# Kernel optimization log

Hardware: AMD Instinct MI355X
Metric: run time of the kernel (lower is better)

The kernel has to match this reference:

```python
import jax, jax.numpy as jnp
import numpy as np
import math

B, S, H = 4, 1024, 1024
E, TOP_K, WINDOW = 4, 2, 64
CONFIGS = [(8, 'standard'), (12, 'standard'), (8, 'linear'), (8, 'local')]
PARAM_NAMES = ['Wq', 'bq', 'Wk', 'bk', 'Wv', 'bv', 'Wo', 'bo']


def setup_inputs() -> dict:
    key = jax.random.key(0)
    ks = jax.random.split(key, 2 + 8 * E)
    d = {}
    d['x'] = jax.random.normal(ks[0], (B, S, H), jnp.float32)
    d['Wg'] = jax.random.normal(ks[1], (H, E), jnp.float32) * 0.02
    i = 2
    for e, (nh, _) in enumerate(CONFIGS):
        hd = H // nh
        pd = nh * hd  # 1020 for nh=12, else 1024
        shapes = [(H, pd), (pd,), (H, pd), (pd,), (H, pd), (pd,), (pd, H), (H,)]
        for nm, shp in zip(PARAM_NAMES, shapes):
            d[f'e{e}_{nm}'] = jax.random.normal(ks[i], shp, jnp.float32) * 0.02
            i += 1
    d['attention_mask'] = jnp.ones((B, S), jnp.int32)
    return d


def _heads(y, nh, hd):
    b, s, _ = y.shape
    return y.reshape(b, s, nh, hd).transpose(0, 2, 1, 3)  # [b, nh, s, hd]


def _attention_expert(x, mask, Wq, bq, Wk, bk, Wv, bv, Wo, bo, nh, atype):
    b, s, _ = x.shape
    hd = Wq.shape[1] // nh
    scale = math.sqrt(hd)
    q = _heads(x @ Wq + bq, nh, hd)
    k = _heads(x @ Wk + bk, nh, hd)
    v = _heads(x @ Wv + bv, nh, hd)
    if atype == 'linear':
        # kernel-trick linear attention; original ignores attention_mask here
        q = jax.nn.elu(q) + 1.0
        k = jax.nn.elu(k) + 1.0
        kv = jnp.einsum('bhsd,bhse->bhde', k, v)
        num = jnp.einsum('bhqd,bhde->bhqe', q, kv)
        den = jnp.einsum('bhqd,bhd->bhq', q, k.sum(axis=2)) + 1e-6
        out = num / den[..., None]
    else:
        scores = jnp.einsum('bhqd,bhkd->bhqk', q, k) / scale
        if atype == 'local':
            idx = jnp.arange(s)
            dist = idx[None, :] - idx[:, None]  # j - i
            local_mask = jnp.abs(dist) <= WINDOW // 2
            scores = jnp.where(local_mask[None, None], scores, -jnp.inf)
        scores = jnp.where(mask[:, None, None, :] == 0, -jnp.inf, scores)
        probs = jax.nn.softmax(scores, axis=-1)
        probs = jnp.where(jnp.isnan(probs), 0.0, probs)  # nan_to_num(nan=0)
        out = jnp.einsum('bhqk,bhkd->bhqd', probs, v)
    out = out.transpose(0, 2, 1, 3).reshape(b, s, -1)
    return out @ Wo + bo


def _forward(x, Wg, eparams, attention_mask):
    b, s, h = x.shape
    # TopKGating (eval mode: no noise). logits -> top_k -> softmax over selected
    logits = x.reshape(-1, h) @ Wg  # [b*s, E]
    top_vals, top_idx = jax.lax.top_k(logits, TOP_K)
    gate_w = jax.nn.softmax(top_vals, axis=-1).reshape(b, s, TOP_K)
    sel = top_idx.reshape(b, s, TOP_K)
    outs = jnp.stack([
        _attention_expert(x, attention_mask, *eparams[e], CONFIGS[e][0], CONFIGS[e][1])
        for e in range(E)
    ], axis=0)  # [E, b, s, h]
    perm = outs.transpose(1, 2, 0, 3)  # [b, s, E, h]
    selected = jnp.take_along_axis(perm, sel[..., None], axis=2)  # [b, s, K, h]
    return (selected * gate_w[..., None]).sum(axis=2)


def reference(x, Wg,
              e0_Wq, e0_bq, e0_Wk, e0_bk, e0_Wv, e0_bv, e0_Wo, e0_bo,
              e1_Wq, e1_bq, e1_Wk, e1_bk, e1_Wv, e1_bv, e1_Wo, e1_bo,
              e2_Wq, e2_bq, e2_Wk, e2_bk, e2_Wv, e2_bv, e2_Wo, e2_bo,
              e3_Wq, e3_bq, e3_Wk, e3_bk, e3_Wv, e3_bv, e3_Wo, e3_bo,
              attention_mask):
    eparams = [
        (e0_Wq, e0_bq, e0_Wk, e0_bk, e0_Wv, e0_bv, e0_Wo, e0_bo),
        (e1_Wq, e1_bq, e1_Wk, e1_bk, e1_Wv, e1_bv, e1_Wo, e1_bo),
        (e2_Wq, e2_bq, e2_Wk, e2_bk, e2_Wv, e2_bv, e2_Wo, e2_bo),
        (e3_Wq, e3_bq, e3_Wk, e3_bk, e3_Wv, e3_bv, e3_Wo, e3_bo),
    ]
    return _forward(x, Wg, eparams, attention_mask)
```

## Files before the change

### kernel.cpp

```cpp
#include <hip/hip_runtime.h>
#include <cmath>

#define B_ 4
#define S_ 1024
#define H_ 1024

typedef short bf16x8 __attribute__((ext_vector_type(8)));
typedef float f32x4 __attribute__((ext_vector_type(4)));
typedef _Float16 half4 __attribute__((ext_vector_type(4)));

__device__ __forceinline__ unsigned short f2bf(float f) {
  unsigned u = __float_as_uint(f);
  u += 0x7fff + ((u >> 16) & 1);
  return (unsigned short)(u >> 16);
}
__device__ __forceinline__ float bf2f(unsigned short h) {
  return __uint_as_float(((unsigned)h) << 16);
}
__device__ __forceinline__ void gld16(const void* g, void* l) {
  __builtin_amdgcn_global_load_lds(
      (const __attribute__((address_space(1))) unsigned int*)g,
      (__attribute__((address_space(3))) unsigned int*)l, 16, 0, 0);
}

__global__ __launch_bounds__(64) void gate_kernel(
    const float* __restrict__ x, const float* __restrict__ Wg,
    float* __restrict__ gw) {
  int t = blockIdx.x;
  int lane = threadIdx.x;
  const float* xr = x + (size_t)t * H_;
  float a0 = 0.f, a1 = 0.f, a2 = 0.f, a3 = 0.f;
  for (int h = lane; h < H_; h += 64) {
    float xv = xr[h];
    const float* wr = Wg + h * 4;
    a0 += xv * wr[0]; a1 += xv * wr[1]; a2 += xv * wr[2]; a3 += xv * wr[3];
  }
  for (int off = 32; off > 0; off >>= 1) {
    a0 += __shfl_down(a0, off);
    a1 += __shfl_down(a1, off);
    a2 += __shfl_down(a2, off);
    a3 += __shfl_down(a3, off);
  }
  if (lane == 0) {
    float v[4] = {a0, a1, a2, a3};
    int i0 = 0; float b0 = v[0];
    for (int e = 1; e < 4; ++e) if (v[e] > b0) { b0 = v[e]; i0 = e; }
    int i1 = -1; float b1 = -INFINITY;
    for (int e = 0; e < 4; ++e) { if (e == i0) continue; if (v[e] > b1) { b1 = v[e]; i1 = e; } }
    float e1v = expf(b1 - b0);
    float w0 = 1.f / (1.f + e1v);
    float w1 = e1v / (1.f + e1v);
    float o[4] = {0.f, 0.f, 0.f, 0.f};
    o[i0] = w0; o[i1] = w1;
    float* g = gw + t * 4;
    g[0] = o[0]; g[1] = o[1]; g[2] = o[2]; g[3] = o[3];
  }
}

__global__ __launch_bounds__(256) void conv_kernel(
    const float* __restrict__ src, unsigned short* __restrict__ dst,
    int nsrc, int ldsrc) {
  int idx = blockIdx.x * 256 + threadIdx.x;
  int m = idx >> 10, c = idx & 1023;
  dst[idx] = (c < nsrc) ? f2bf(src[(size_t)m * ldsrc + c]) : (unsigned short)0;
}

__global__ __launch_bounds__(256) void wtrans4_kernel(
    const float* __restrict__ s0, const float* __restrict__ s1,
    const float* __restrict__ s2, const float* __restrict__ s3,
    unsigned short* __restrict__ d0, unsigned short* __restrict__ d1,
    unsigned short* __restrict__ d2, unsigned short* __restrict__ d3, int pd) {
  __shared__ float tile[32][33];
  int z = blockIdx.z;
  const float* src = (z == 0) ? s0 : (z == 1) ? s1 : (z == 2) ? s2 : s3;
  unsigned short* dst = (z == 0) ? d0 : (z == 1) ? d1 : (z == 2) ? d2 : d3;
  int ksrc = (z < 3) ? 1024 : pd;
  int nsrc = (z < 3) ? pd : 1024;
  int ldsrc = (z < 3) ? pd : 1024;
  int k0 = blockIdx.x * 32, n0 = blockIdx.y * 32;
  int tx = threadIdx.x & 31, ty = threadIdx.x >> 5;
  for (int i = 0; i < 32; i += 8) {
    int k = k0 + ty + i, n = n0 + tx;
    tile[ty + i][tx] = (k < ksrc && n < nsrc) ? src[(size_t)k * ldsrc + n] : 0.f;
  }
  __syncthreads();
  for (int i = 0; i < 32; i += 8) {
    int n = n0 + ty + i, k = k0 + tx;
    dst[(size_t)n * 1024 + k] = f2bf(tile[tx][ty + i]);
  }
}

__global__ __launch_bounds__(256) void gemm_mfma(
    const unsigned short* __restrict__ A, const unsigned short* __restrict__ Bt,
    const float* __restrict__ b0, const float* __restrict__ b1,
    const float* __restrict__ b2, void* __restrict__ Cv, int ldc,
    int nact, int elu_ncut, int out_bf16, int mode,
    const float* __restrict__ gw, int expert, int remap,
    int qs_ncut, float qscale) {
  constexpr int K = 1024;
  __shared__ __align__(16) unsigned short As[128 * 32];
  __shared__ __align__(16) unsigned short Bs[128 * 32];
  int tid = threadIdx.x, wave = tid >> 6, lane = tid & 63;
  int quad = lane >> 4, lrow = lane & 15;
  int rw = (wave >> 1) * 64, cw = (wave & 1) * 64;
  int m0 = blockIdx.y * 128, n0 = blockIdx.x * 128;
  int srow = wave * 32 + (lane >> 2);
  int scol = (lane & 3) * 8;
  const unsigned short* gA = A + (size_t)(m0 + srow) * K + scol;
  const unsigned short* gB = Bt + (size_t)(n0 + srow) * K + scol;
  unsigned short* lA = &As[wave * 1024];
  unsigned short* lB = &Bs[wave * 1024];
  f32x4 acc[4][4];
#pragma unroll
  for (int mt = 0; mt < 4; ++mt)
#pragma unroll
    for (int nt = 0; nt < 4; ++nt) acc[mt][nt] = (f32x4){0.f, 0.f, 0.f, 0.f};

  for (int k0 = 0; k0 < K; k0 += 32) {
    gld16(gA + k0, lA);
    gld16(gA + 16 * K + k0, lA + 512);
    gld16(gB + k0, lB);
    gld16(gB + 16 * K + k0, lB + 512);
    __syncthreads();
    bf16x8 af[4], bfr[4];
#pragma unroll
    for (int t = 0; t < 4; ++t) {
      af[t]  = *(const bf16x8*)&As[(rw + t * 16 + lrow) * 32 + quad * 8];
      bfr[t] = *(const bf16x8*)&Bs[(cw + t * 16 + lrow) * 32 + quad * 8];
    }
#pragma unroll
    for (int mt = 0; mt < 4; ++mt)
#pragma unroll
      for (int nt = 0; nt < 4; ++nt)
        acc[mt][nt] = __builtin_amdgcn_mfma_f32_16x16x32_bf16(
            af[mt], bfr[nt], acc[mt][nt], 0, 0, 0);
    __syncthreads();
  }
#pragma unroll
  for (int nt = 0; nt < 4; ++nt) {
    int n = n0 + cw + nt * 16 + lrow;
    int slice = n >> 10, noff = n & 1023;
    if (noff >= nact) continue;
    const float* bp = (slice == 0) ? b0 : (slice == 1) ? b1 : b2;
    float bias = bp[noff];
    bool do_elu = n < elu_ncut;
    bool do_qs = n < qs_ncut;
    int col = n;
    if (remap) {
      int head = (noff * 12337) >> 20;
      col = slice * 1152 + head * 96 + (noff - head * 85);
    }
#pragma unroll
    for (int mt = 0; mt < 4; ++mt) {
      int mb = m0 + rw + mt * 16 + quad * 4;
#pragma unroll
      for (int r = 0; r < 4; ++r) {
        int m = mb + r;
        float val = acc[mt][nt][r] + bias;
        if (do_elu) val = (val > 0.f) ? val + 1.f : expf(val);
        if (do_qs) val *= qscale;
        size_t ci = (size_t)m * ldc + col;
        if (out_bf16) {
          ((unsigned short*)Cv)[ci] = f2bf(val);
        } else {
          float* C = (float*)Cv;
          if (mode == 0) C[ci] = val;
          else {
            float g = gw[m * 4 + expert];
            if (mode == 1) C[ci] = g * val;
            else           C[ci] += g * val;
          }
        }
      }
    }
  }
}

struct OutP {
  const unsigned short* A[4];
  const unsigned short* B[4];
  const float* bias[4];
};

__global__ __launch_bounds__(256) void gemm_out4(
    OutP p, const float* __restrict__ gw, float* __restrict__ part) {
  constexpr int K = 1024;
  __shared__ __align__(16) unsigned short As[128 * 32];
  __shared__ __align__(16) unsigned short Bs[128 * 32];
  int e = blockIdx.z;
  const unsigned short* A = p.A[e];
  const unsigned short* Bt = p.B[e];
  const float* bp = p.bias[e];
  float* C = part + (size_t)e * (4096ull * 1024ull);
  int tid = threadIdx.x, wave = tid >> 6, lane = tid & 63;
  int quad = lane >> 4, lrow = lane & 15;
  int rw = (wave >> 1) * 64, cw = (wave & 1) * 64;
  int m0 = blockIdx.y * 128, n0 = blockIdx.x * 128;
  int srow = wave * 32 + (lane >> 2);
  int scol = (lane & 3) * 8;
  const unsigned short* gA = A + (size_t)(m0 + srow) * K + scol;
  const unsigned short* gB = Bt + (size_t)(n0 + srow) * K + scol;
  unsigned short* lA = &As[wave * 1024];
  unsigned short* lB = &Bs[wave * 1024];
  f32x4 acc[4][4];
#pragma unroll
  for (int mt = 0; mt < 4; ++mt)
#pragma unroll
    for (int nt = 0; nt < 4; ++nt) acc[mt][nt] = (f32x4){0.f, 0.f, 0.f, 0.f};

  for (int k0 = 0; k0 < K; k0 += 32) {
    gld16(gA + k0, lA);
    gld16(gA + 16 * K + k0, lA + 512);
    gld16(gB + k0, lB);
    gld16(gB + 16 * K + k0, lB + 512);
    __syncthreads();
    bf16x8 af[4], bfr[4];
#pragma unroll
    for (int t = 0; t < 4; ++t) {
      af[t]  = *(const bf16x8*)&As[(rw + t * 16 + lrow) * 32 + quad * 8];
      bfr[t] = *(const bf16x8*)&Bs[(cw + t * 16 + lrow) * 32 + quad * 8];
    }
#pragma unroll
    for (int mt = 0; mt < 4; ++mt)
#pragma unroll
      for (int nt = 0; nt < 4; ++nt)
        acc[mt][nt] = __builtin_amdgcn_mfma_f32_16x16x32_bf16(
            af[mt], bfr[nt], acc[mt][nt], 0, 0, 0);
    __syncthreads();
  }
#pragma unroll
  for (int nt = 0; nt < 4; ++nt) {
    int n = n0 + cw + nt * 16 + lrow;
    float bias = bp[n];
#pragma unroll
    for (int mt = 0; mt < 4; ++mt) {
      int mb = m0 + rw + mt * 16 + quad * 4;
#pragma unroll
      for (int r = 0; r < 4; ++r) {
        int m = mb + r;
        float g = gw[m * 4 + e];
        C[(size_t)m * 1024 + n] = g * (acc[mt][nt][r] + bias);
      }
    }
  }
}

__global__ __launch_bounds__(256) void reduce4(
    const float* __restrict__ part, float* __restrict__ out) {
  constexpr size_t N = 4096ull * 1024ull;
  size_t idx = ((size_t)blockIdx.x * 256 + threadIdx.x) * 4;
  f32x4 a0 = *(const f32x4*)(part + idx);
  f32x4 a1 = *(const f32x4*)(part + idx + N);
  f32x4 a2 = *(const f32x4*)(part + idx + 2 * N);
  f32x4 a3 = *(const f32x4*)(part + idx + 3 * N);
  f32x4 s;
#pragma unroll
  for (int j = 0; j < 4; ++j) {
    float t = a0[j];
    t += a1[j]; t += a2[j]; t += a3[j];
    s[j] = t;
  }
  *(f32x4*)(out + idx) = s;
}

__global__ __launch_bounds__(256) void padzero(
    unsigned short* __restrict__ qkv1, unsigned short* __restrict__ aob1) {
  int idx = blockIdx.x * 256 + threadIdx.x;
  int m = idx / 396, r = idx % 396;
  int slice = r / 132, r2 = r % 132;
  int head = r2 / 11, c = 85 + r2 % 11;
  qkv1[(size_t)m * 3456 + slice * 1152 + head * 96 + c] = 0;
  if (idx < 4096 * 4) {
    int mm = idx >> 2, cc = 1020 + (idx & 3);
    aob1[(size_t)mm * 1024 + cc] = 0;
  }
}

template <int HD, bool LOCAL>
__device__ __forceinline__ void attn_body(
    char* smem,
    const unsigned short* __restrict__ q, const unsigned short* __restrict__ k,
    const unsigned short* __restrict__ v, const int* __restrict__ amask,
    unsigned short* __restrict__ ao, int ldq, int h) {
  constexpr int HDP = (HD + 31) & ~31;
  constexpr int DCH = HDP / 32;
  constexpr int NDT = HDP / 16;
  constexpr int NCH = HDP / 8;
  constexpr int QT = 256, KT = 64;
  constexpr int KLD = HDP + 8;
  constexpr int VLD = KT + 4;
  constexpr int W2 = 32;
  unsigned short* Ks = (unsigned short*)smem;
  _Float16* Vt = (_Float16*)(smem + (size_t)KT * KLD * 2);
  unsigned long long* amq =
      (unsigned long long*)(smem + (size_t)KT * KLD * 2 + (size_t)HDP * VLD * 2);
  int tid = threadIdx.x, wave = tid >> 6, lane = tid & 63;
  int quad = lane >> 4, l15 = lane & 15;
  int q0 = blockIdx.x * QT, b = blockIdx.z;
  size_t baseq = ((size_t)b * S_) * ldq + (size_t)h * HDP;
  size_t baseo = ((size_t)b * S_) * H_ + (size_t)h * HD;

  {
    unsigned long long bb0 = __ballot(amask[b * S_ + wave * 128 + lane] != 0);
    unsigned long long bb1 = __ballot(amask[b * S_ + wave * 128 + 64 + lane] != 0);
    if (lane == 0) { amq[wave * 2] = bb0; amq[wave * 2 + 1] = bb1; }
  }

  int qrow[2];
  bf16x8 qf[2][DCH];
#pragma unroll
  for (int g = 0; g < 2; ++g) {
    qrow[g] = q0 + wave * 32 + g * 16 + l15;
#pragma unroll
    for (int c = 0; c < DCH; ++c)
#pragma unroll
      for (int j = 0; j < 8; ++j) {
        int d = c * 32 + quad * 8 + j;
        qf[g][c][j] =
            (d < HD) ? (short)q[baseq + (size_t)qrow[g] * ldq + d] : (short)0;
      }
  }

  int jlo = 0, jhi = S_;
  if (LOCAL) {
    jlo = q0 - W2; if (jlo < 0) jlo = 0; jlo &= ~(KT - 1);
    jhi = q0 + QT + W2; if (jhi > S_) jhi = S_;
  }

  int skey = tid & 63, sc8a = tid >> 6, sc8b = 8 + (tid >> 6);
  bool sactb = sc8b < NCH;
  const unsigned short* kg = k + baseq + (size_t)skey * ldq;
  const unsigned short* vg = v + baseq + (size_t)skey * ldq;
  bf16x8 kra = {}, krb = {}, vra = {}, vrb = {};
  {
    size_t o = (size_t)jlo * ldq;
    kra = *(const bf16x8*)(kg + o + sc8a * 8);
    vra = *(const bf16x8*)(vg + o + sc8a * 8);
    if (sactb) {
      krb = *(const bf16x8*)(kg + o + sc8b * 8);
      vrb = *(const bf16x8*)(vg + o + sc8b * 8);
    }
  }

  float m_run[2] = {-1e30f, -1e30f}, l_run[2] = {0.f, 0.f};
  f32x4 accd[2][NDT];
#pragma unroll
  for (int g = 0; g < 2; ++g)
#pragma unroll
    for (int dt = 0; dt < NDT; ++dt) accd[g][dt] = (f32x4){0.f, 0.f, 0.f, 0.f};

  for (int j0 = jlo; j0 < jhi; j0 += KT) {
    __syncthreads();
    *(bf16x8*)&Ks[skey * KLD + sc8a * 8] = kra;
#pragma unroll
    for (int j = 0; j < 8; ++j)
      Vt[(sc8a * 8 + j) * VLD + skey] = (_Float16)bf2f((unsigned short)vra[j]);
    if (sactb) {
      *(bf16x8*)&Ks[skey * KLD + sc8b * 8] = krb;
#pragma unroll
      for (int j = 0; j < 8; ++j)
        Vt[(sc8b * 8 + j) * VLD + skey] = (_Float16)bf2f((unsigned short)vrb[j]);
    }
    __syncthreads();
    int jn = j0 + KT;
    if (jn < jhi) {
      size_t o = (size_t)jn * ldq;
      kra = *(const bf16x8*)(kg + o + sc8a * 8);
      vra = *(const bf16x8*)(vg + o + sc8a * 8);
      if (sactb) {
        krb = *(const bf16x8*)(kg + o + sc8b * 8);
        vrb = *(const bf16x8*)(vg + o + sc8b * 8);
      }
    }
    f32x4 sf[2][4];
#pragma unroll
    for (int kt = 0; kt < 4; ++kt) {
      sf[0][kt] = (f32x4){0.f, 0.f, 0.f, 0.f};
      sf[1][kt] = (f32x4){0.f, 0.f, 0.f, 0.f};
#pragma unroll
      for (int c = 0; c < DCH; ++c) {
        bf16x8 kf = *(const bf16x8*)&Ks[(kt * 16 + l15) * KLD + c * 32 + quad * 8];
        sf[0][kt] = __builtin_amdgcn_mfma_f32_16x16x32_bf16(kf, qf[0][c], sf[0][kt], 0, 0, 0);
        sf[1][kt] = __builtin_amdgcn_mfma_f32_16x16x32_bf16(kf, qf[1][c], sf[1][kt], 0, 0, 0);
      }
    }
    unsigned long long mb = amq[j0 >> 6];
    unsigned mw[2] = {(unsigned)mb, (unsigned)(mb >> 32)};
    float pvv[2][4][4];
    float mx[2] = {-1e30f, -1e30f};
#pragma unroll
    for (int kt = 0; kt < 4; ++kt) {
      unsigned word = mw[kt >> 1];
      int sh = (kt & 1) * 16 + quad * 4;
#pragma unroll
      for (int r = 0; r < 4; ++r) {
        bool okm = (word >> (sh + r)) & 1;
#pragma unroll
        for (int g = 0; g < 2; ++g) {
          bool ok = okm;
          if (LOCAL) {
            int dj = (j0 + kt * 16 + quad * 4 + r) - qrow[g];
            ok = ok && (dj <= W2) && (dj >= -W2);
          }
          float s = ok ? sf[g][kt][r] : -1e30f;
          pvv[g][kt][r] = s;
          mx[g] = fmaxf(mx[g], s);
        }
      }
    }
    half4 pf[2][4];
    float aR[2][4];
#pragma unroll
    for (int g = 0; g < 2; ++g) {
      float mxg = fmaxf(mx[g], __shfl_xor(mx[g], 16));
      mxg = fmaxf(mxg, __shfl_xor(mxg, 32));
      float m_new = fmaxf(m_run[g], mxg);
      float psum = 0.f;
#pragma unroll
      for (int kt = 0; kt < 4; ++kt)
#pragma unroll
        for (int r = 0; r < 4; ++r) {
          float s = pvv[g][kt][r];
          float p = (s > -1e29f) ? __builtin_amdgcn_exp2f(s - m_new) : 0.f;
          pvv[g][kt][r] = p;
          psum += p;
        }
      psum += __shfl_xor(psum, 16);
      psum += __shfl_xor(psum, 32);
      float alpha = __builtin_amdgcn_exp2f(m_run[g] - m_new);
      m_run[g] = m_new;
      l_run[g] = l_run[g] * alpha + psum;
#pragma unroll
      for (int r = 0; r < 4; ++r)
        aR[g][r] = __shfl(alpha, (lane & 48) | (quad * 4 + r));
#pragma unroll
      for (int dt = 0; dt < NDT; ++dt)
#pragma unroll
        for (int r = 0; r < 4; ++r) accd[g][dt][r] *= aR[g][r];
#pragma unroll
      for (int kt = 0; kt < 4; ++kt)
#pragma unroll
        for (int r = 0; r < 4; ++r) pf[g][kt][r] = (_Float16)pvv[g][kt][r];
    }
#pragma unroll
    for (int dt = 0; dt < NDT; ++dt)
#pragma unroll
      for (int kt = 0; kt < 4; ++kt) {
        half4 vf = *(const half4*)&Vt[(dt * 16 + l15) * VLD + kt * 16 + quad * 4];
        accd[0][dt] = __builtin_amdgcn_mfma_f32_16x16x16f16(pf[0][kt], vf, accd[0][dt], 0, 0, 0);
        accd[1][dt] = __builtin_amdgcn_mfma_f32_16x16x16f16(pf[1][kt], vf, accd[1][dt], 0, 0, 0);
      }
  }
#pragma unroll
  for (int g = 0; g < 2; ++g) {
    float linv = (l_run[g] > 0.f) ? 1.f / l_run[g] : 0.f;
    float lR[4];
#pragma unroll
    for (int r = 0; r < 4; ++r)
      lR[r] = __shfl(linv, (lane & 48) | (quad * 4 + r));
#pragma unroll
    for (int dt = 0; dt < NDT; ++dt) {
      int d = dt * 16 + l15;
      if (d >= HD) continue;
#pragma unroll
      for (int r = 0; r < 4; ++r) {
        int row = q0 + wave * 32 + g * 16 + quad * 4 + r;
        ao[baseo + (size_t)row * H_ + d] = f2bf(accd[g][dt][r] * lR[r]);
      }
    }
  }
}

template <int HD, bool LOCAL>
__global__ __launch_bounds__(512) void attn_mfma3(
    const unsigned short* __restrict__ q, const unsigned short* __restrict__ k,
    const unsigned short* __restrict__ v, const int* __restrict__ amask,
    unsigned short* __restrict__ ao, int ldq) {
  constexpr int HDP = (HD + 31) & ~31;
  __shared__ __align__(16) char smem[64 * (HDP + 8) * 2 + HDP * 68 * 2 + 128];
  attn_body<HD, LOCAL>(smem, q, k, v, amask, ao, ldq, blockIdx.y);
}

__global__ __launch_bounds__(512) void attn_mega(
    const unsigned short* __restrict__ qkv0,
    const unsigned short* __restrict__ qkv1,
    const unsigned short* __restrict__ qkv3, const int* __restrict__ amask,
    unsigned short* __restrict__ ao0, unsigned short* __restrict__ ao1,
    unsigned short* __restrict__ ao3) {
  __shared__ __align__(16) char smem[34944];
  int y = blockIdx.y;
  if (y < 8)
    attn_body<128, false>(smem, qkv0, qkv0 + 1024, qkv0 + 2048, amask, ao0,
                          3072, y);
  else if (y < 20)
    attn_body<85, false>(smem, qkv1, qkv1 + 1152, qkv1 + 2304, amask, ao1,
                         3456, y - 8);
  else
    attn_body<128, true>(smem, qkv3, qkv3 + 1024, qkv3 + 2048, amask, ao3,
                         3072, y - 20);
}

#define NSPLIT 4
__global__ __launch_bounds__(256) void linkv_mfma(
    const unsigned short* __restrict__ k, const unsigned short* __restrict__ v,
    float* __restrict__ kvp, float* __restrict__ ksump, int ld) {
  constexpr int HD = 128;
  constexpr int TLD = 34;
  __shared__ __align__(16) unsigned short Kt[HD * TLD];
  __shared__ __align__(16) unsigned short Vt[HD * TLD];
  int h = blockIdx.x, b = blockIdx.y, split = blockIdx.z;
  int bh = b * 8 + h;
  int tid = threadIdx.x, wave = tid >> 6, lane = tid & 63;
  int quad = lane >> 4, l15 = lane & 15;
  int rw = (wave >> 1) * 64, cw = (wave & 1) * 64;
  size_t base = ((size_t)b * S_) * ld + (size_t)h * HD;
  int s_begin = split * (S_ / NSPLIT);

  f32x4 acc[4][4];
#pragma unroll
  for (int mt = 0; mt < 4; ++mt)
#pragma unroll
    for (int nt = 0; nt < 4; ++nt) acc[mt][nt] = (f32x4){0.f, 0.f, 0.f, 0.f};
  float ksacc = 0.f;
  int myd = tid & 127, half = tid >> 7;

  for (int c0 = 0; c0 < S_ / NSPLIT; c0 += 32) {
    for (int idx = tid; idx < 32 * HD; idx += 256) {
      int d = idx & 127, s = idx >> 7;
      size_t g = base + (size_t)(s_begin + c0 + s) * ld + d;
      Kt[d * TLD + s] = k[g];
      Vt[d * TLD + s] = v[g];
    }
    __syncthreads();
    bf16x8 af[4], bf[4];
#pragma unroll
    for (int t = 0; t < 4; ++t) {
      af[t] = *(const bf16x8*)&Vt[(rw + t * 16 + l15) * TLD + quad * 8];
      bf[t] = *(const bf16x8*)&Kt[(cw + t * 16 + l15) * TLD + quad * 8];
    }
#pragma unroll
    for (int mt = 0; mt < 4; ++mt)
#pragma unroll
      for (int nt = 0; nt < 4; ++nt)
        acc[mt][nt] = __builtin_amdgcn_mfma_f32_16x16x32_bf16(
            af[mt], bf[nt], acc[mt][nt], 0, 0, 0);
#pragma unroll
    for (int s = 0; s < 16; ++s)
      ksacc += bf2f(Kt[myd * TLD + half * 16 + s]);
    __syncthreads();
  }
  float* red = (float*)Kt;
  if (half == 1) red[myd] = ksacc;
  __syncthreads();
  if (half == 0)
    ksump[((size_t)split * 32 + bh) * HD + myd] = ksacc + red[myd];
  float* kvo = kvp + ((size_t)split * 32 + bh) * (HD * HD);
#pragma unroll
  for (int mt = 0; mt < 4; ++mt)
#pragma unroll
    for (int nt = 0; nt < 4; ++nt) {
      int dk = cw + nt * 16 + l15;
#pragma unroll
      for (int r = 0; r < 4; ++r) {
        int dv = rw + mt * 16 + quad * 4 + r;
        kvo[(size_t)dv * HD + dk] = acc[mt][nt][r];
      }
    }
}

__global__ __launch_bounds__(256) void linkv_reduce(
    const float* __restrict__ kvp, const float* __restrict__ ksump,
    unsigned short* __restrict__ kvb, float* __restrict__ ksum) {
  int idx = blockIdx.x * 256 + threadIdx.x;
  float s = 0.f;
#pragma unroll
  for (int p = 0; p < NSPLIT; ++p) s += kvp[(size_t)p * (32 * 128 * 128) + idx];
  kvb[idx] = f2bf(s);
  if (idx < 32 * 128) {
    float t = 0.f;
#pragma unroll
    for (int p = 0; p < NSPLIT; ++p) t += ksump[(size_t)p * (32 * 128) + idx];
    ksum[idx] = t;
  }
}

__global__ __launch_bounds__(256) void linattn_mfma(
    const unsigned short* __restrict__ q, const unsigned short* __restrict__ kvT,
    const float* __restrict__ ksum, unsigned short* __restrict__ ao, int ldq) {
  constexpr int KLD = 136;
  __shared__ __align__(16) unsigned short Ks[128 * KLD];
  __shared__ float ksL[128];
  int tid = threadIdx.x, wave = tid >> 6, lane = tid & 63;
  int quad = lane >> 4, l15 = lane & 15;
  int rw = (wave >> 1) * 64, cw = (wave & 1) * 64;
  int q0 = blockIdx.x * 128, h = blockIdx.y, b = blockIdx.z;
  int bh = b * 8 + h;
  size_t baseq = ((size_t)b * S_) * ldq + (size_t)h * 128;
  size_t baseo = ((size_t)b * S_) * H_ + (size_t)h * 128;
  const unsigned short* kvg = kvT + (size_t)bh * (128 * 128);
  for (int idx = tid; idx < 128 * 16; idx += 256) {
    int e = idx >> 4, c = idx & 15;
    *(bf16x8*)&Ks[e * KLD + c * 8] = *(const bf16x8*)&kvg[e * 128 + c * 8];
  }
  if (tid < 128) ksL[tid] = ksum[(size_t)bh * 128 + tid];
  bf16x8 qf[4][4];
#pragma unroll
  for (int mt = 0; mt < 4; ++mt) {
    const unsigned short* qr = q + baseq + (size_t)(q0 + rw + mt * 16 + l15) * ldq;
#pragma unroll
    for (int kc = 0; kc < 4; ++kc)
      qf[mt][kc] = *(const bf16x8*)&qr[kc * 32 + quad * 8];
  }
  __syncthreads();
  f32x4 acc[4][4];
#pragma unroll
  for (int mt = 0; mt < 4; ++mt)
#pragma unroll
    for (int nt = 0; nt < 4; ++nt) acc[mt][nt] = (f32x4){0.f, 0.f, 0.f, 0.f};
#pragma unroll
  for (int kc = 0; kc < 4; ++kc) {
    bf16x8 bf[4];
#pragma unroll
    for (int nt = 0; nt < 4; ++nt)
      bf[nt] = *(const bf16x8*)&Ks[(cw + nt * 16 + l15) * KLD + kc * 32 + quad * 8];
#pragma unroll
    for (int mt = 0; mt < 4; ++mt)
#pragma unroll
      for (int nt = 0; nt < 4; ++nt)
        acc[mt][nt] = __builtin_amdgcn_mfma_f32_16x16x32_bf16(
            qf[mt][kc], bf[nt], acc[mt][nt], 0, 0, 0);
  }
  float den[4];
#pragma unroll
  for (int mt = 0; mt < 4; ++mt) {
    float s = 0.f;
#pragma unroll
    for (int kc = 0; kc < 4; ++kc)
#pragma unroll
      for (int j = 0; j < 8; ++j)
        s += bf2f((unsigned short)qf[mt][kc][j]) * ksL[kc * 32 + quad * 8 + j];
    s += __shfl_xor(s, 16);
    s += __shfl_xor(s, 32);
    den[mt] = s;
  }
#pragma unroll
  for (int mt = 0; mt < 4; ++mt)
#pragma unroll
    for (int r = 0; r < 4; ++r) {
      float dv = __shfl(den[mt], (lane & 48) | (quad * 4 + r));
      float inv = 1.f / (dv + 1e-6f);
      int row = q0 + rw + mt * 16 + quad * 4 + r;
#pragma unroll
      for (int nt = 0; nt < 4; ++nt) {
        int col = cw + nt * 16 + l15;
        ao[baseo + (size_t)row * H_ + col] = f2bf(acc[mt][nt][r] * inv);
      }
    }
}

extern "C" void kernel_launch(void* const* d_in, const int* in_sizes, int n_in,
                              void* d_out, int out_size, void* d_ws, size_t ws_size,
                              hipStream_t stream) {
  const float* x = (const float*)d_in[0];
  const float* Wg = (const float*)d_in[1];
  const int* amask = (const int*)d_in[34];
  float* out = (float*)d_out;
  char* ws = (char*)d_ws;
  const size_t MiB = 1ull << 20;
  const int nhs[4] = {8, 12, 8, 8};
  const float LOG2E = 1.4426950408889634f;

  if (ws_size >= 157 * MiB) {
    float* gw = (float*)ws;
    float* ksum = (float*)(ws + (64ull << 10));
    unsigned short* kvb = (unsigned short*)(ws + 1 * MiB);
    unsigned short* xb = (unsigned short*)(ws + 4 * MiB);
    float* kvp = (float*)(ws + 4 * MiB);
    unsigned short* qkvT = (unsigned short*)(ws + 12 * MiB);
    float* ksump = (float*)(ws + 12 * MiB);
    unsigned short* woT[4];
    for (int e = 0; e < 4; ++e)
      woT[e] = (unsigned short*)(ws + (18 + 2 * e) * MiB);
    const size_t qkvOff[4] = {26 * MiB, 50 * MiB, 77 * MiB, 101 * MiB};
    unsigned short* qkvE[4];
    for (int e = 0; e < 4; ++e) qkvE[e] = (unsigned short*)(ws + qkvOff[e]);
    float* part = (float*)(ws + 26 * MiB);
    unsigned short* aobE[4];
    for (int e = 0; e < 4; ++e)
      aobE[e] = (unsigned short*)(ws + (125 + 8 * e) * MiB);

    conv_kernel<<<16384, 256, 0, stream>>>(x, xb, 1024, 1024);
    gate_kernel<<<4096, 64, 0, stream>>>(x, Wg, gw);
    padzero<<<6336, 256, 0, stream>>>(qkvE[1], aobE[1]);

    for (int e = 0; e < 4; ++e) {
      const float* Wq = (const float*)d_in[2 + 8 * e + 0];
      const float* bq = (const float*)d_in[2 + 8 * e + 1];
      const float* Wk = (const float*)d_in[2 + 8 * e + 2];
      const float* bk = (const float*)d_in[2 + 8 * e + 3];
      const float* Wv = (const float*)d_in[2 + 8 * e + 4];
      const float* bv = (const float*)d_in[2 + 8 * e + 5];
      const float* Wo = (const float*)d_in[2 + 8 * e + 6];
      int nh = nhs[e];
      int hd = H_ / nh;
      int pd = nh * hd;
      int ldqkv = (e == 1) ? 3456 : 3072;
      int qs_ncut = (e == 2) ? 0 : 1024;
      float qscale = LOG2E / sqrtf((float)hd);

      wtrans4_kernel<<<dim3(32, 32, 4), 256, 0, stream>>>(
          Wq, Wk, Wv, Wo, qkvT, qkvT + (1 << 20), qkvT + (2 << 20), woT[e], pd);

      gemm_mfma<<<dim3(24, 32), 256, 0, stream>>>(
          xb, qkvT, bq, bk, bv, qkvE[e], ldqkv,
          (pd == 1020) ? 1020 : 1024, (e == 2) ? 2048 : 0, 1, 0, nullptr, 0,
          (e == 1) ? 1 : 0, qs_ncut, qscale);
    }

    linkv_mfma<<<dim3(8, B_, NSPLIT), 256, 0, stream>>>(
        qkvE[2] + 1024, qkvE[2] + 2048, kvp, ksump, 3072);
    linkv_reduce<<<(32 * 128 * 128) / 256, 256, 0, stream>>>(kvp, ksump, kvb, ksum);
    linattn_mfma<<<dim3(S_ / 128, 8, B_), 256, 0, stream>>>(
        qkvE[2], kvb, ksum, aobE[2], 3072);

    attn_mega<<<dim3(S_ / 256, 28, B_), 512, 0, stream>>>(
        qkvE[0], qkvE[1], qkvE[3], amask, aobE[0], aobE[1], aobE[3]);

    OutP p;
    for (int e = 0; e < 4; ++e) {
      p.A[e] = aobE[e];
      p.B[e] = woT[e];
      p.bias[e] = (const float*)d_in[2 + 8 * e + 7];
    }
    gemm_out4<<<dim3(8, 32, 4), 256, 0, stream>>>(p, gw, part);
    reduce4<<<4096, 256, 0, stream>>>(part, out);
    return;
  }

  float* gw            = (float*)(ws + 0);
  unsigned short* kvb  = (unsigned short*)(ws + (1ull << 20));
  float* ksum          = (float*)(ws + (3ull << 20) + (1ull << 19));
  unsigned short* xb   = (unsigned short*)(ws + (4ull << 20));
  unsigned short* qkvT = (unsigned short*)(ws + (12ull << 20));
  unsigned short* woT  = (unsigned short*)(ws + (18ull << 20));
  unsigned short* qkv  = (unsigned short*)(ws + (20ull << 20));
  unsigned short* aob  = (unsigned short*)(ws + (49ull << 20));
  float* kvp           = (float*)(ws + (57ull << 20));
  float* ksump         = (float*)(ws + (73ull << 20));

  conv_kernel<<<16384, 256, 0, stream>>>(x, xb, 1024, 1024);
  gate_kernel<<<4096, 64, 0, stream>>>(x, Wg, gw);

  for (int e = 0; e < 4; ++e) {
    const float* Wq = (const float*)d_in[2 + 8 * e + 0];
    const float* bq = (const float*)d_in[2 + 8 * e + 1];
    const float* Wk = (const float*)d_in[2 + 8 * e + 2];
    const float* bk = (const float*)d_in[2 + 8 * e + 3];
    const float* Wv = (const float*)d_in[2 + 8 * e + 4];
    const float* bv = (const float*)d_in[2 + 8 * e + 5];
    const float* Wo = (const float*)d_in[2 + 8 * e + 6];
    const float* bo = (const float*)d_in[2 + 8 * e + 7];
    int nh = nhs[e];
    int hd = H_ / nh;
    int pd = nh * hd;
    int ldqkv = (e == 1) ? 3456 : 3072;
    int qs_ncut = (e == 2) ? 0 : 1024;
    float qscale = LOG2E / sqrtf((float)hd);

    wtrans4_kernel<<<dim3(32, 32, 4), 256, 0, stream>>>(
        Wq, Wk, Wv, Wo, qkvT, qkvT + (1 << 20), qkvT + (2 << 20), woT, pd);

    gemm_mfma<<<dim3(24, 32), 256, 0, stream>>>(
        xb, qkvT, bq, bk, bv, qkv, ldqkv,
        (pd == 1020) ? 1020 : 1024, (e == 2) ? 2048 : 0, 1, 0, nullptr, 0,
        (e == 1) ? 1 : 0, qs_ncut, qscale);

    if (e == 2) {
      const unsigned short* qb = qkv;
      const unsigned short* kb = qkv + 1024;
      const unsigned short* vb = qkv + 2048;
      linkv_mfma<<<dim3(8, B_, NSPLIT), 256, 0, stream>>>(kb, vb, kvp, ksump, 3072);
      linkv_reduce<<<(32 * 128 * 128) / 256, 256, 0, stream>>>(kvp, ksump, kvb, ksum);
      linattn_mfma<<<dim3(S_ / 128, 8, B_), 256, 0, stream>>>(qb, kvb, ksum, aob, 3072);
    } else if (e == 1) {
      attn_mfma3<85, false><<<dim3(S_ / 256, 12, B_), 512, 0, stream>>>(
          qkv, qkv + 1152, qkv + 2304, amask, aob, 3456);
    } else if (e == 3) {
      attn_mfma3<128, true><<<dim3(S_ / 256, 8, B_), 512, 0, stream>>>(
          qkv, qkv + 1024, qkv + 2048, amask, aob, 3072);
    } else {
      attn_mfma3<128, false><<<dim3(S_ / 256, 8, B_), 512, 0, stream>>>(
          qkv, qkv + 1024, qkv + 2048, amask, aob, 3072);
    }

    gemm_mfma<<<dim3(8, 32), 256, 0, stream>>>(
        aob, woT, bo, bo, bo, out, 1024, 1024, 0, 0, (e == 0) ? 1 : 2, gw, e, 0,
        0, 1.0f);
  }
}
```

Baseline: 593.6 us.

## Batch weight transposes and QKV GEMMs across experts; double-buffer attention K/V tiles

The per-expert loop of weight-transpose and QKV GEMM launches is replaced by one 16-slice transpose kernel and one batched QKV GEMM whose grid z-dimension indexes the expert. This cuts launch count and fills the GPU with more blocks per launch. The attention body now double-buffers its K/V shared-memory tiles, writing the next tile while computing on the current one, so only one barrier per iteration remains. This doubles shared memory per block, which may reduce occupancy, and the transposed weights now share workspace with the attention-output buffers, which are written later.

```diff
diff --git a/kernel.cpp b/kernel.cpp
--- a/kernel.cpp
+++ b/kernel.cpp
@@ -77,6 +77,34 @@
   int ksrc = (z < 3) ? 1024 : pd;
   int nsrc = (z < 3) ? pd : 1024;
   int ldsrc = (z < 3) ? pd : 1024;
+  int k0 = blockIdx.x * 32, n0 = blockIdx.y * 32;
+  int tx = threadIdx.x & 31, ty = threadIdx.x >> 5;
+  for (int i = 0; i < 32; i += 8) {
+    int k = k0 + ty + i, n = n0 + tx;
+    tile[ty + i][tx] = (k < ksrc && n < nsrc) ? src[(size_t)k * ldsrc + n] : 0.f;
+  }
+  __syncthreads();
+  for (int i = 0; i < 32; i += 8) {
+    int n = n0 + ty + i, k = k0 + tx;
+    dst[(size_t)n * 1024 + k] = f2bf(tile[tx][ty + i]);
+  }
+}
+
+struct W16 {
+  const float* src[16];
+  unsigned short* dst[16];
+  int pd[4];
+};
+__global__ __launch_bounds__(256) void wtrans16_kernel(W16 p) {
+  __shared__ float tile[32][33];
+  int z = blockIdx.z;
+  int e = z >> 2, m = z & 3;
+  const float* src = p.src[z];
+  unsigned short* dst = p.dst[z];
+  int pd = p.pd[e];
+  int ksrc = (m < 3) ? 1024 : pd;
+  int nsrc = (m < 3) ? pd : 1024;
+  int ldsrc = (m < 3) ? pd : 1024;
   int k0 = blockIdx.x * 32, n0 = blockIdx.y * 32;
   int tx = threadIdx.x & 31, ty = threadIdx.x >> 5;
   for (int i = 0; i < 32; i += 8) {
@@ -176,6 +204,95 @@
   }
 }
 
+struct QkvP {
+  const unsigned short* Bt[4];
+  const float* bq[4];
+  const float* bk[4];
+  const float* bv[4];
+  unsigned short* C[4];
+  int ldc[4];
+  int nact[4];
+  int elu_ncut[4];
+  int remap[4];
+  int qs_ncut[4];
+  float qscale[4];
+};
+__global__ __launch_bounds__(256) void gemm_qkv4(
+    const unsigned short* __restrict__ A, QkvP p) {
+  constexpr int K = 1024;
+  __shared__ __align__(16) unsigned short As[128 * 32];
+  __shared__ __align__(16) unsigned short Bs[128 * 32];
+  int e = blockIdx.z;
+  const unsigned short* Bt = p.Bt[e];
+  unsigned short* Cv = p.C[e];
+  int ldc = p.ldc[e], nact = p.nact[e], elu_ncut = p.elu_ncut[e];
+  int remap = p.remap[e], qs_ncut = p.qs_ncut[e];
+  float qscale = p.qscale[e];
+  int tid = threadIdx.x, wave = tid >> 6, lane = tid & 63;
+  int quad = lane >> 4, lrow = lane & 15;
+  int rw = (wave >> 1) * 64, cw = (wave & 1) * 64;
+  int m0 = blockIdx.y * 128, n0 = blockIdx.x * 128;
+  int srow = wave * 32 + (lane >> 2);
+  int scol = (lane & 3) * 8;
+  const unsigned short* gA = A + (size_t)(m0 + srow) * K + scol;
+  const unsigned short* gB = Bt + (size_t)(n0 + srow) * K + scol;
+  unsigned short* lA = &As[wave * 1024];
+  unsigned short* lB = &Bs[wave * 1024];
+  f32x4 acc[4][4];
+#pragma unroll
+  for (int mt = 0; mt < 4; ++mt)
+#pragma unroll
+    for (int nt = 0; nt < 4; ++nt) acc[mt][nt] = (f32x4){0.f, 0.f, 0.f, 0.f};
+
+  for (int k0 = 0; k0 < K; k0 += 32) {
+    gld16(gA + k0, lA);
+    gld16(gA + 16 * K + k0, lA + 512);
+    gld16(gB + k0, lB);
+    gld16(gB + 16 * K + k0, lB + 512);
+    __syncthreads();
+    bf16x8 af[4], bfr[4];
+#pragma unroll
+    for (int t = 0; t < 4; ++t) {
+      af[t]  = *(const bf16x8*)&As[(rw + t * 16 + lrow) * 32 + quad * 8];
+      bfr[t] = *(const bf16x8*)&Bs[(cw + t * 16 + lrow) * 32 + quad * 8];
+    }
+#pragma unroll
+    for (int mt = 0; mt < 4; ++mt)
+#pragma unroll
+      for (int nt = 0; nt < 4; ++nt)
+        acc[mt][nt] = __builtin_amdgcn_mfma_f32_16x16x32_bf16(
+            af[mt], bfr[nt], acc[mt][nt], 0, 0, 0);
+    __syncthreads();
+  }
+#pragma unroll
+  for (int nt = 0; nt < 4; ++nt) {
+    int n = n0 + cw + nt * 16 + lrow;
+    int slice = n >> 10, noff = n & 1023;
+    if (noff >= nact) continue;
+    const float* bp = (slice == 0) ? p.bq[e] : (slice == 1) ? p.bk[e] : p.bv[e];
+    float bias = bp[noff];
+    bool do_elu = n < elu_ncut;
+    bool do_qs = n < qs_ncut;
+    int col = n;
+    if (remap) {
+      int head = (noff * 12337) >> 20;
+      col = slice * 1152 + head * 96 + (noff - head * 85);
+    }
+#pragma unroll
+    for (int mt = 0; mt < 4; ++mt) {
+      int mb = m0 + rw + mt * 16 + quad * 4;
+#pragma unroll
+      for (int r = 0; r < 4; ++r) {
+        int m = mb + r;
+        float val = acc[mt][nt][r] + bias;
+        if (do_elu) val = (val > 0.f) ? val + 1.f : expf(val);
+        if (do_qs) val *= qscale;
+        Cv[(size_t)m * ldc + col] = f2bf(val);
+      }
+    }
+  }
+}
+
 struct OutP {
   const unsigned short* A[4];
   const unsigned short* B[4];
@@ -290,10 +407,12 @@
   constexpr int KLD = HDP + 8;
   constexpr int VLD = KT + 4;
   constexpr int W2 = 32;
+  constexpr int KSZ = KT * KLD;
+  constexpr int VSZ = HDP * VLD;
   unsigned short* Ks = (unsigned short*)smem;
-  _Float16* Vt = (_Float16*)(smem + (size_t)KT * KLD * 2);
+  _Float16* Vt = (_Float16*)(smem + 2 * KSZ * 2);
   unsigned long long* amq =
-      (unsigned long long*)(smem + (size_t)KT * KLD * 2 + (size_t)HDP * VLD * 2);
+      (unsigned long long*)(smem + 2 * KSZ * 2 + 2 * VSZ * 2);
   int tid = threadIdx.x, wave = tid >> 6, lane = tid & 63;
   int quad = lane >> 4, l15 = lane & 15;
   int q0 = blockIdx.x * QT, b = blockIdx.z;
@@ -342,15 +461,7 @@
     }
   }
 
-  float m_run[2] = {-1e30f, -1e30f}, l_run[2] = {0.f, 0.f};
-  f32x4 accd[2][NDT];
-#pragma unroll
-  for (int g = 0; g < 2; ++g)
-#pragma unroll
-    for (int dt = 0; dt < NDT; ++dt) accd[g][dt] = (f32x4){0.f, 0.f, 0.f, 0.f};
-
-  for (int j0 = jlo; j0 < jhi; j0 += KT) {
-    __syncthreads();
+  {
     *(bf16x8*)&Ks[skey * KLD + sc8a * 8] = kra;
 #pragma unroll
     for (int j = 0; j < 8; ++j)
@@ -361,7 +472,18 @@
       for (int j = 0; j < 8; ++j)
         Vt[(sc8b * 8 + j) * VLD + skey] = (_Float16)bf2f((unsigned short)vrb[j]);
     }
-    __syncthreads();
+  }
+  int cur = 0;
+  __syncthreads();
+
+  float m_run[2] = {-1e30f, -1e30f}, l_run[2] = {0.f, 0.f};
+  f32x4 accd[2][NDT];
+#pragma unroll
+  for (int g = 0; g < 2; ++g)
+#pragma unroll
+    for (int dt = 0; dt < NDT; ++dt) accd[g][dt] = (f32x4){0.f, 0.f, 0.f, 0.f};
+
+  for (int j0 = jlo; j0 < jhi; j0 += KT) {
     int jn = j0 + KT;
     if (jn < jhi) {
       size_t o = (size_t)jn * ldq;
@@ -372,6 +494,8 @@
         vrb = *(const bf16x8*)(vg + o + sc8b * 8);
       }
     }
+    const unsigned short* KsR = Ks + cur * KSZ;
+    const _Float16* VtR = Vt + cur * VSZ;
     f32x4 sf[2][4];
 #pragma unroll
     for (int kt = 0; kt < 4; ++kt) {
@@ -379,7 +503,7 @@
       sf[1][kt] = (f32x4){0.f, 0.f, 0.f, 0.f};
 #pragma unroll
       for (int c = 0; c < DCH; ++c) {
-        bf16x8 kf = *(const bf16x8*)&Ks[(kt * 16 + l15) * KLD + c * 32 + quad * 8];
+        bf16x8 kf = *(const bf16x8*)&KsR[(kt * 16 + l15) * KLD + c * 32 + quad * 8];
         sf[0][kt] = __builtin_amdgcn_mfma_f32_16x16x32_bf16(kf, qf[0][c], sf[0][kt], 0, 0, 0);
         sf[1][kt] = __builtin_amdgcn_mfma_f32_16x16x32_bf16(kf, qf[1][c], sf[1][kt], 0, 0, 0);
       }
@@ -442,14 +566,30 @@
 #pragma unroll
         for (int r = 0; r < 4; ++r) pf[g][kt][r] = (_Float16)pvv[g][kt][r];
     }
+    if (jn < jhi) {
+      unsigned short* KsW = Ks + (cur ^ 1) * KSZ;
+      _Float16* VtW = Vt + (cur ^ 1) * VSZ;
+      *(bf16x8*)&KsW[skey * KLD + sc8a * 8] = kra;
+#pragma unroll
+      for (int j = 0; j < 8; ++j)
+        VtW[(sc8a * 8 + j) * VLD + skey] = (_Float16)bf2f((unsigned short)vra[j]);
+      if (sactb) {
+        *(bf16x8*)&KsW[skey * KLD + sc8b * 8] = krb;
+#pragma unroll
+        for (int j = 0; j < 8; ++j)
+          VtW[(sc8b * 8 + j) * VLD + skey] = (_Float16)bf2f((unsigned short)vrb[j]);
+      }
+    }
 #pragma unroll
     for (int dt = 0; dt < NDT; ++dt)
 #pragma unroll
       for (int kt = 0; kt < 4; ++kt) {
-        half4 vf = *(const half4*)&Vt[(dt * 16 + l15) * VLD + kt * 16 + quad * 4];
+        half4 vf = *(const half4*)&VtR[(dt * 16 + l15) * VLD + kt * 16 + quad * 4];
         accd[0][dt] = __builtin_amdgcn_mfma_f32_16x16x16f16(pf[0][kt], vf, accd[0][dt], 0, 0, 0);
         accd[1][dt] = __builtin_amdgcn_mfma_f32_16x16x16f16(pf[1][kt], vf, accd[1][dt], 0, 0, 0);
       }
+    __syncthreads();
+    cur ^= 1;
   }
 #pragma unroll
   for (int g = 0; g < 2; ++g) {
@@ -477,7 +617,7 @@
     const unsigned short* __restrict__ v, const int* __restrict__ amask,
     unsigned short* __restrict__ ao, int ldq) {
   constexpr int HDP = (HD + 31) & ~31;
-  __shared__ __align__(16) char smem[64 * (HDP + 8) * 2 + HDP * 68 * 2 + 128];
+  __shared__ __align__(16) char smem[2 * 64 * (HDP + 8) * 2 + 2 * HDP * 68 * 2 + 128];
   attn_body<HD, LOCAL>(smem, q, k, v, amask, ao, ldq, blockIdx.y);
 }
 
@@ -487,7 +627,7 @@
     const unsigned short* __restrict__ qkv3, const int* __restrict__ amask,
     unsigned short* __restrict__ ao0, unsigned short* __restrict__ ao1,
     unsigned short* __restrict__ ao3) {
-  __shared__ __align__(16) char smem[34944];
+  __shared__ __align__(16) char smem[69760];
   int y = blockIdx.y;
   if (y < 8)
     attn_body<128, false>(smem, qkv0, qkv0 + 1024, qkv0 + 2048, amask, ao0,
@@ -676,7 +816,6 @@
     unsigned short* kvb = (unsigned short*)(ws + 1 * MiB);
     unsigned short* xb = (unsigned short*)(ws + 4 * MiB);
     float* kvp = (float*)(ws + 4 * MiB);
-    unsigned short* qkvT = (unsigned short*)(ws + 12 * MiB);
     float* ksump = (float*)(ws + 12 * MiB);
     unsigned short* woT[4];
     for (int e = 0; e < 4; ++e)
@@ -688,34 +827,42 @@
     unsigned short* aobE[4];
     for (int e = 0; e < 4; ++e)
       aobE[e] = (unsigned short*)(ws + (125 + 8 * e) * MiB);
+    unsigned short* qkvT4 = (unsigned short*)(ws + 125 * MiB);
 
     conv_kernel<<<16384, 256, 0, stream>>>(x, xb, 1024, 1024);
     gate_kernel<<<4096, 64, 0, stream>>>(x, Wg, gw);
+
+    W16 w;
+    for (int e = 0; e < 4; ++e) {
+      w.pd[e] = nhs[e] * (H_ / nhs[e]);
+      for (int m = 0; m < 3; ++m) {
+        w.src[e * 4 + m] = (const float*)d_in[2 + 8 * e + 2 * m];
+        w.dst[e * 4 + m] = qkvT4 + (size_t)(e * 3 + m) * (1 << 20);
+      }
+      w.src[e * 4 + 3] = (const float*)d_in[2 + 8 * e + 6];
+      w.dst[e * 4 + 3] = woT[e];
+    }
+    wtrans16_kernel<<<dim3(32, 32, 16), 256, 0, stream>>>(w);
+
+    QkvP qp;
+    for (int e = 0; e < 4; ++e) {
+      int hd = H_ / nhs[e];
+      int pd = nhs[e] * hd;
+      qp.Bt[e] = qkvT4 + (size_t)(e * 3) * (1 << 20);
+      qp.bq[e] = (const float*)d_in[2 + 8 * e + 1];
+      qp.bk[e] = (const float*)d_in[2 + 8 * e + 3];
+      qp.bv[e] = (const float*)d_in[2 + 8 * e + 5];
+      qp.C[e] = qkvE[e];
+      qp.ldc[e] = (e == 1) ? 3456 : 3072;
+      qp.nact[e] = (pd == 1020) ? 1020 : 1024;
+      qp.elu_ncut[e] = (e == 2) ? 2048 : 0;
+      qp.remap[e] = (e == 1) ? 1 : 0;
+      qp.qs_ncut[e] = (e == 2) ? 0 : 1024;
+      qp.qscale[e] = LOG2E / sqrtf((float)hd);
+    }
+    gemm_qkv4<<<dim3(24, 32, 4), 256, 0, stream>>>(xb, qp);
+
     padzero<<<6336, 256, 0, stream>>>(qkvE[1], aobE[1]);
-
-    for (int e = 0; e < 4; ++e) {
-      const float* Wq = (const float*)d_in[2 + 8 * e + 0];
-      const float* bq = (const float*)d_in[2 + 8 * e + 1];
-      const float* Wk = (const float*)d_in[2 + 8 * e + 2];
-      const float* bk = (const float*)d_in[2 + 8 * e + 3];
-      const float* Wv = (const float*)d_in[2 + 8 * e + 4];
-      const float* bv = (const float*)d_in[2 + 8 * e + 5];
-      const float* Wo = (const float*)d_in[2 + 8 * e + 6];
-      int nh = nhs[e];
-      int hd = H_ / nh;
-      int pd = nh * hd;
-      int ldqkv = (e == 1) ? 3456 : 3072;
-      int qs_ncut = (e == 2) ? 0 : 1024;
-      float qscale = LOG2E / sqrtf((float)hd);
-
-      wtrans4_kernel<<<dim3(32, 32, 4), 256, 0, stream>>>(
-          Wq, Wk, Wv, Wo, qkvT, qkvT + (1 << 20), qkvT + (2 << 20), woT[e], pd);
-
-      gemm_mfma<<<dim3(24, 32), 256, 0, stream>>>(
-          xb, qkvT, bq, bk, bv, qkvE[e], ldqkv,
-          (pd == 1020) ? 1020 : 1024, (e == 2) ? 2048 : 0, 1, 0, nullptr, 0,
-          (e == 1) ? 1 : 0, qs_ncut, qscale);
-    }
 
     linkv_mfma<<<dim3(8, B_, NSPLIT), 256, 0, stream>>>(
         qkvE[2] + 1024, qkvE[2] + 2048, kvp, ksump, 3072);
```

New measurement: 578.0 us. 1.03x faster.
